# Performance work log

Measured on AMD Instinct MI355X. Metric: run time of the kernel, lower is better.

## Reference

```python
import jax, jax.numpy as jnp
import numpy as np

N, F, H, C, E = 100000, 512, 128, 8, 1600000
GAMMA = 1.0
EPS = 1e-8


def _xavier(key, shape):
    a = np.sqrt(6.0 / (shape[0] + shape[1])).astype(np.float32)
    return jax.random.uniform(key, shape, jnp.float32, -a, a)


def _agg(w, x, src, dst):
    # y[i] = sum_{e: dst[e]==i} w[e] * x[src[e]]  (sparse adj @ x)
    return jax.ops.segment_sum(w[:, None] * x[src], dst, num_segments=N)


def setup_inputs() -> dict:
    key = jax.random.key(0)
    ks = jax.random.split(key, 8)
    features = jax.random.normal(ks[0], (N, F), jnp.float32)
    edge_src = jax.random.randint(ks[1], (E,), 0, N)
    edge_dst = jax.random.randint(ks[2], (E,), 0, N)
    # degree-based normalized edge weights, mimicking D^p A D^p
    deg = jnp.zeros((N,), jnp.float32).at[edge_dst].add(1.0)
    deg = jnp.maximum(deg, 1.0)
    d_half = deg ** -0.5
    d_one = deg ** -1.0
    w1 = d_half[edge_dst] * d_half[edge_src]   # D^-1/2 A D^-1/2
    w2 = d_one[edge_dst] * d_one[edge_src]     # D^-1  A D^-1
    Wm1 = _xavier(ks[3], (F, H))
    Ws1 = _xavier(ks[4], (F, H))
    Wm2 = _xavier(ks[5], (H, C))
    Ws2 = _xavier(ks[6], (H, C))
    noise = jax.random.normal(ks[7], (N, C), jnp.float32)
    return {"features": features, "edge_src": edge_src, "edge_dst": edge_dst,
            "w1": w1, "w2": w2, "Wm1": Wm1, "Ws1": Ws1, "Wm2": Wm2,
            "Ws2": Ws2, "noise": noise}


def reference(features, edge_src, edge_dst, w1, w2, Wm1, Ws1, Wm2, Ws2, noise):
    # GGCL_F (eval mode: dropout is identity)
    miu1 = jax.nn.elu(features @ Wm1)
    sigma1 = jax.nn.relu(features @ Ws1)
    att1 = jnp.exp(-GAMMA * sigma1)
    miu_h = _agg(w1, miu1 * att1, edge_src, edge_dst)
    sigma_h = _agg(w2, sigma1 * att1 * att1, edge_src, edge_dst)
    # GGCL_D
    miu2 = jax.nn.elu(miu_h @ Wm2)
    sigma2 = jax.nn.relu(sigma_h @ Ws2)
    att2 = jnp.exp(-GAMMA * sigma2)
    mean_out = _agg(w1, miu2 * att2, edge_src, edge_dst)
    # GGCL_D returns (mean_out, sigma2); reparameterized sample
    return mean_out + noise * jnp.sqrt(sigma2 + EPS)
```

## Files before the change

### kernel.cpp

```cpp
#include <hip/hip_runtime.h>
#include <cstdint>

#define AS1 __attribute__((address_space(1)))
#define AS3 __attribute__((address_space(3)))

typedef __attribute__((ext_vector_type(8))) short short8;
typedef __attribute__((ext_vector_type(4))) float floatx4;
typedef unsigned short u16;

static constexpr int NN   = 100000;
static constexpr int FF   = 512;
static constexpr int HH   = 128;
static constexpr int EE   = 1600000;
static constexpr int PADM = 100096;
static constexpr int NPAD = 100352;
static constexpr int NB   = 98;

__device__ __forceinline__ u16 f2bf_rne(float v) {
    uint32_t u = __builtin_bit_cast(uint32_t, v);
    u += 0x7fffu + ((u >> 16) & 1u);
    return (u16)(u >> 16);
}
__device__ __forceinline__ float bf2f(u16 h) {
    uint32_t u = ((uint32_t)h) << 16;
    return __builtin_bit_cast(float, u);
}
__device__ __forceinline__ void async16(const void* g, void* l) {
    __builtin_amdgcn_global_load_lds((AS1 const void*)g, (AS3 void*)l, 16, 0, 0);
}

__global__ void k_split_w(const float* __restrict__ Wm1, const float* __restrict__ Ws1,
                          u16* __restrict__ whi, u16* __restrict__ wlo) {
    int t = blockIdx.x * 256 + threadIdx.x;
    int n = t >> 9, k = t & 511;
    float v = (n < HH) ? Wm1[k * HH + n] : Ws1[k * HH + (n - HH)];
    u16 h = f2bf_rne(v);
    whi[t] = h;
    wlo[t] = f2bf_rne(v - bf2f(h));
}

__global__ void k_prep_w2(const float* __restrict__ Wm2, const float* __restrict__ Ws2,
                          u16* __restrict__ W2B) {
    int t = blockIdx.x * 256 + threadIdx.x;
    int j = t & 7, l = (t >> 3) & 63, kc = (t >> 9) & 3, p = t >> 11;
    int n = l & 15, quad = l >> 4;
    int k = kc * 32 + quad * 8 + j;
    float v = 0.f;
    if (n < 8) {
        float wv = (p == 0) ? Wm2[k * 8 + n] : Ws2[k * 8 + n];
        v = (p == 2) ? (wv - bf2f(f2bf_rne(wv))) : wv;
    }
    W2B[t] = f2bf_rne(v);
}

__global__ void k_deg(const int* __restrict__ dst, int* __restrict__ deg) {
    int e = blockIdx.x * 256 + threadIdx.x;
    atomicAdd(&deg[dst[e]], 1);
}
__global__ void k_dh(const int* __restrict__ deg, float2* __restrict__ dd) {
    int t = blockIdx.x * 256 + threadIdx.x;
    int d = max(deg[t], 1);
    float df = (float)d;
    dd[t] = make_float2(1.f / sqrtf(df), 1.f / df);
}

__global__ __launch_bounds__(512, 4) void k_gemm(
        const float* __restrict__ A,
        const u16* __restrict__ BhiG, const u16* __restrict__ BloG,
        const u16* __restrict__ W2B, const float2* __restrict__ dd,
        float* __restrict__ Z) {
    __shared__ u16 sm[24576];
    const int tid = threadIdx.x;
    const int w = tid >> 6, lane = tid & 63;
    const int ml = lane & 15, quad = lane >> 4;
    const int wrow = w & 1, wcol = w >> 1;
    const int rowBase = blockIdx.x * 128;

    floatx4 am[4][2], as_[4][2];
#pragma unroll
    for (int i = 0; i < 4; i++)
#pragma unroll
        for (int j = 0; j < 2; j++) {
            am[i][j]  = (floatx4){0.f, 0.f, 0.f, 0.f};
            as_[i][j] = (floatx4){0.f, 0.f, 0.f, 0.f};
        }

    const int r0 = tid >> 2, ko = (tid & 3) * 8;
    const int arow = min(rowBase + r0, NN - 1);
    const float* gA = A + (size_t)arow * FF + ko;
    const u16* gBh = BhiG + (size_t)r0 * FF + ko;
    const u16* gBl = BloG + (size_t)(128 + r0) * FF + ko;

    const int aoff = (wrow * 64 + ml) * 32 + quad * 8;
    const int bmo  = 8192  + (32 * wcol + ml) * 32 + quad * 8;
    const int bso  = 12288 + (32 * wcol + ml) * 32 + quad * 8;
    const int blo_ = 16384 + (32 * wcol + ml) * 32 + quad * 8;

    for (int kt = 0; kt < FF; kt += 32) {
        __syncthreads();
        async16(gBh + kt,                      &sm[8192  + tid * 8]);
        async16(gBh + (size_t)128 * FF + kt,   &sm[12288 + tid * 8]);
        async16(gBl + kt,                      &sm[16384 + tid * 8]);
        {
            const float4* pA = (const float4*)(gA + kt);
            float4 x0 = pA[0], x1 = pA[1];
            float xv[8] = {x0.x, x0.y, x0.z, x0.w, x1.x, x1.y, x1.z, x1.w};
            short8 hv, lv;
#pragma unroll
            for (int q = 0; q < 8; q++) {
                u16 hh = f2bf_rne(xv[q]);
                hv[q] = (short)hh;
                lv[q] = (short)f2bf_rne(xv[q] - bf2f(hh));
            }
            *(short8*)&sm[tid * 8] = hv;
            *(short8*)&sm[4096 + tid * 8] = lv;
        }
        __syncthreads();

        short8 ah[4], al[4];
#pragma unroll
        for (int i = 0; i < 4; i++) ah[i] = *(const short8*)&sm[aoff + i * 512];
#pragma unroll
        for (int i = 0; i < 4; i++) al[i] = *(const short8*)&sm[4096 + aoff + i * 512];
#pragma unroll
        for (int jm = 0; jm < 2; jm++) {
            short8 b = *(const short8*)&sm[bmo + jm * 512];
#pragma unroll
            for (int i = 0; i < 4; i++)
                am[i][jm] = __builtin_amdgcn_mfma_f32_16x16x32_bf16(ah[i], b, am[i][jm], 0, 0, 0);
        }
#pragma unroll
        for (int js = 0; js < 2; js++) {
            short8 bh = *(const short8*)&sm[bso + js * 512];
            short8 bl = *(const short8*)&sm[blo_ + js * 512];
#pragma unroll
            for (int i = 0; i < 4; i++) {
                floatx4 c = as_[i][js];
                c = __builtin_amdgcn_mfma_f32_16x16x32_bf16(ah[i], bh, c, 0, 0, 0);
                c = __builtin_amdgcn_mfma_f32_16x16x32_bf16(ah[i], bl, c, 0, 0, 0);
                c = __builtin_amdgcn_mfma_f32_16x16x32_bf16(al[i], bh, c, 0, 0, 0);
                as_[i][js] = c;
            }
        }
    }

    short8 wm[4], wsh[4], wsl[4];
#pragma unroll
    for (int kc = 0; kc < 4; kc++) {
        wm[kc]  = *(const short8*)&W2B[(kc * 64 + lane) * 8];
        wsh[kc] = *(const short8*)&W2B[2048 + (kc * 64 + lane) * 8];
        wsl[kc] = *(const short8*)&W2B[4096 + (kc * 64 + lane) * 8];
    }
    const int rg = w & 1, pp = w >> 1;

#pragma unroll
    for (int h = 0; h < 4; h++) {
        __syncthreads();
        if (wrow == (h >> 1)) {
#pragma unroll
            for (int ii = 0; ii < 2; ii++) {
                int i = (h & 1) * 2 + ii;
#pragma unroll
                for (int jm = 0; jm < 2; jm++) {
                    int c = 32 * wcol + 16 * jm + ml;
#pragma unroll
                    for (int r = 0; r < 4; r++) {
                        int lr = ii * 16 + quad * 4 + r;
                        float2 d2 = dd[rowBase + h * 32 + lr];
                        float u = am[i][jm][r], v = as_[i][jm][r];
                        float m1 = u > 0.f ? u : __expf(u) - 1.f;
                        float s1 = v > 0.f ? v : 0.f;
                        float a1 = __expf(-s1);
                        float xmv = d2.x * m1 * a1;
                        float xsv = d2.y * s1 * a1 * a1;
                        u16 hh = f2bf_rne(xsv);
                        sm[lr * 136 + c]        = f2bf_rne(xmv);
                        sm[4352 + lr * 136 + c] = hh;
                        sm[8704 + lr * 136 + c] = f2bf_rne(xsv - bf2f(hh));
                    }
                }
            }
        }
        __syncthreads();
        if (w < 4) {
            floatx4 z = (floatx4){0.f, 0.f, 0.f, 0.f};
#pragma unroll
            for (int kc = 0; kc < 4; kc++) {
                if (pp == 0) {
                    short8 a = *(const short8*)&sm[(rg * 16 + ml) * 136 + kc * 32 + quad * 8];
                    z = __builtin_amdgcn_mfma_f32_16x16x32_bf16(a, wm[kc], z, 0, 0, 0);
                } else {
                    short8 a = *(const short8*)&sm[4352 + (rg * 16 + ml) * 136 + kc * 32 + quad * 8];
                    short8 b = *(const short8*)&sm[8704 + (rg * 16 + ml) * 136 + kc * 32 + quad * 8];
                    z = __builtin_amdgcn_mfma_f32_16x16x32_bf16(a, wsh[kc], z, 0, 0, 0);
                    z = __builtin_amdgcn_mfma_f32_16x16x32_bf16(a, wsl[kc], z, 0, 0, 0);
                    z = __builtin_amdgcn_mfma_f32_16x16x32_bf16(b, wsh[kc], z, 0, 0, 0);
                }
            }
            if (ml < 8) {
                int rowb = rowBase + h * 32 + rg * 16 + quad * 4;
#pragma unroll
                for (int r = 0; r < 4; r++)
                    if (rowb + r < NN) Z[(size_t)(rowb + r) * 16 + pp * 8 + ml] = z[r];
            }
        }
    }
}

__global__ void k_scan1(const int* __restrict__ deg, int* __restrict__ bsum) {
    int t = threadIdx.x;
    int4 v = ((const int4*)deg)[blockIdx.x * 256 + t];
    __shared__ int red[256];
    red[t] = v.x + v.y + v.z + v.w;
    __syncthreads();
    for (int o = 128; o > 0; o >>= 1) {
        if (t < o) red[t] += red[t + o];
        __syncthreads();
    }
    if (t == 0) bsum[blockIdx.x] = red[0];
}

__global__ void k_scan2(const int* __restrict__ bsum, int* __restrict__ boff) {
    int t = threadIdx.x;
    __shared__ int s[128];
    int own = (t < NB) ? bsum[t] : 0;
    s[t] = own;
    __syncthreads();
    for (int o = 1; o < 128; o <<= 1) {
        int v = (t >= o) ? s[t - o] : 0;
        __syncthreads();
        s[t] += v;
        __syncthreads();
    }
    if (t < NB) boff[t] = s[t] - own;
}

__global__ void k_scan3(const int* __restrict__ deg, const int* __restrict__ boff,
                        int* __restrict__ ptr, int* __restrict__ cursor) {
    int t = threadIdx.x;
    int gi = blockIdx.x * 256 + t;
    int4 v = ((const int4*)deg)[gi];
    int tsum = v.x + v.y + v.z + v.w;
    __shared__ int s[256];
    s[t] = tsum;
    __syncthreads();
    for (int o = 1; o < 256; o <<= 1) {
        int pv = (t >= o) ? s[t - o] : 0;
        __syncthreads();
        s[t] += pv;
        __syncthreads();
    }
    int base = boff[blockIdx.x] + (s[t] - tsum);
    int4 e;
    e.x = base;
    e.y = base + v.x;
    e.z = e.y + v.y;
    e.w = e.z + v.z;
    ((int4*)ptr)[gi] = e;
    ((int4*)cursor)[gi] = e;
}

__global__ void k_scatter(const int* __restrict__ src, const int* __restrict__ dst,
                          int* __restrict__ cursor, int* __restrict__ pay) {
    int e = blockIdx.x * 256 + threadIdx.x;
    int d = dst[e];
    int p = atomicAdd(&cursor[d], 1);
    int pr = pay[p];
    asm volatile("" :: "v"(pr) : "memory");
    pay[p] = src[e];
}

__global__ __launch_bounds__(256) void k_aggA(const int* __restrict__ ptr,
        const int* __restrict__ pay, const float* __restrict__ Z,
        const float2* __restrict__ dd, const float* __restrict__ noise,
        float* __restrict__ y, float* __restrict__ out) {
    int wave = threadIdx.x >> 6, lane = threadIdx.x & 63;
    int i = blockIdx.x * 4 + wave;
    if (i >= NN) return;
    int er = lane >> 3, c = lane & 7;
    int s0 = ptr[i], e0 = ptr[i + 1];
    float am = 0.f, as_ = 0.f;
    int j = s0 + er;
    int sidx = (j < e0) ? pay[j] : -1;
    while (sidx >= 0) {
        int jn = j + 8;
        int snext = (jn < e0) ? pay[jn] : -1;
        const float* zr = Z + (size_t)sidx * 16;
        am  += zr[c];
        as_ += zr[8 + c];
        j = jn;
        sidx = snext;
    }
    am  += __shfl_xor(am, 8, 64);
    am  += __shfl_xor(am, 16, 64);
    am  += __shfl_xor(am, 32, 64);
    as_ += __shfl_xor(as_, 8, 64);
    as_ += __shfl_xor(as_, 16, 64);
    as_ += __shfl_xor(as_, 32, 64);
    if (lane < 8) {
        float2 d2 = dd[i];
        float hm = d2.x * am, hs = d2.y * as_;
        float miu2 = hm > 0.f ? hm : __expf(hm) - 1.f;
        float s2 = hs > 0.f ? hs : 0.f;
        y[i * 8 + lane]   = d2.x * miu2 * __expf(-s2);
        out[i * 8 + lane] = noise[i * 8 + lane] * sqrtf(s2 + 1e-8f);
    }
}

__global__ __launch_bounds__(256) void k_aggB(const int* __restrict__ ptr,
        const int* __restrict__ pay, const float* __restrict__ y,
        const float2* __restrict__ dd, float* __restrict__ out) {
    int wave = threadIdx.x >> 6, lane = threadIdx.x & 63;
    int i = blockIdx.x * 4 + wave;
    if (i >= NN) return;
    int er = lane >> 3, c = lane & 7;
    int s0 = ptr[i], e0 = ptr[i + 1];
    float acc = 0.f;
    int j = s0 + er;
    int sidx = (j < e0) ? pay[j] : -1;
    while (sidx >= 0) {
        int jn = j + 8;
        int snext = (jn < e0) ? pay[jn] : -1;
        acc += y[(size_t)sidx * 8 + c];
        j = jn;
        sidx = snext;
    }
    acc += __shfl_xor(acc, 8, 64);
    acc += __shfl_xor(acc, 16, 64);
    acc += __shfl_xor(acc, 32, 64);
    if (lane < 8) out[i * 8 + lane] += dd[i].x * acc;
}

extern "C" void kernel_launch(void* const* d_in, const int* in_sizes, int n_in,
                              void* d_out, int out_size, void* d_ws, size_t ws_size,
                              hipStream_t stream) {
    (void)in_sizes; (void)n_in; (void)out_size; (void)ws_size;
    const float* feat  = (const float*)d_in[0];
    const int*   esrc  = (const int*)d_in[1];
    const int*   edst  = (const int*)d_in[2];
    const float* Wm1   = (const float*)d_in[5];
    const float* Ws1   = (const float*)d_in[6];
    const float* Wm2   = (const float*)d_in[7];
    const float* Ws2   = (const float*)d_in[8];
    const float* noise = (const float*)d_in[9];
    float* out = (float*)d_out;

    char* ws = (char*)d_ws;
    size_t off = 0;
    auto alloc = [&](size_t bytes) -> void* {
        void* p = ws + off;
        off += (bytes + 255) & ~(size_t)255;
        return p;
    };
    u16*    WhiT = (u16*)alloc((size_t)256 * 512 * 2);
    u16*    WloT = (u16*)alloc((size_t)256 * 512 * 2);
    u16*    W2B  = (u16*)alloc((size_t)6144 * 2);
    float*  Z    = (float*)alloc((size_t)NN * 16 * 4);
    float*  yb   = (float*)alloc((size_t)NN * 8 * 4);
    int*    deg  = (int*)alloc((size_t)NPAD * 4);
    float2* dd   = (float2*)alloc((size_t)NPAD * 8);
    int*    ptr  = (int*)alloc((size_t)(NPAD + 4) * 4);
    int*    cur  = (int*)alloc((size_t)NPAD * 4);
    int*    bsum = (int*)alloc(256 * 4);
    int*    boff = (int*)alloc(256 * 4);
    int*    pay  = (int*)alloc((size_t)EE * 4);

    hipMemsetAsync(deg, 0, (size_t)NPAD * 4, stream);

    k_deg    <<<EE / 256, 256, 0, stream>>>(edst, deg);
    k_dh     <<<NPAD / 256, 256, 0, stream>>>(deg, dd);
    k_scan1  <<<NB, 256, 0, stream>>>(deg, bsum);
    k_scan2  <<<1, 128, 0, stream>>>(bsum, boff);
    k_scan3  <<<NB, 256, 0, stream>>>(deg, boff, ptr, cur);
    k_scatter<<<EE / 256, 256, 0, stream>>>(esrc, edst, cur, pay);

    k_split_w<<<512, 256, 0, stream>>>(Wm1, Ws1, WhiT, WloT);
    k_prep_w2<<<24, 256, 0, stream>>>(Wm2, Ws2, W2B);
    k_gemm   <<<PADM / 128, 512, 0, stream>>>(feat, WhiT, WloT, W2B, dd, Z);

    k_aggA<<<(NN + 3) / 4, 256, 0, stream>>>(ptr, pay, Z, dd, noise, yb, out);
    k_aggB<<<(NN + 3) / 4, 256, 0, stream>>>(ptr, pay, yb, dd, out);
}
```

Before: 601.3 us.

## Double-buffer GEMM LDS tiles and XOR-swizzle layout to avoid bank conflicts

The first-layer GEMM main loop now double-buffers its LDS tiles. It prefetches the next K-slice of A into registers and issues async B loads into the alternate buffer while MFMAs run on the current buffer, then drops one barrier per iteration. It also XOR-swizzles the 8-element column chunks in LDS to reduce bank conflicts on the short8 reads. LDS use grows from 48KB to 80KB per block, which may reduce occupancy under the 512x4 launch bound.

Result: slower. 634.1 us (+5.5%).

```diff
diff --git a/kernel.cpp b/kernel.cpp
--- a/kernel.cpp
+++ b/kernel.cpp
@@ -27,6 +27,18 @@
 }
 __device__ __forceinline__ void async16(const void* g, void* l) {
     __builtin_amdgcn_global_load_lds((AS1 const void*)g, (AS3 void*)l, 16, 0, 0);
+}
+__device__ __forceinline__ void cvt_store(float4 x0, float4 x1, u16* dh, u16* dl) {
+    float xv[8] = {x0.x, x0.y, x0.z, x0.w, x1.x, x1.y, x1.z, x1.w};
+    short8 hv, lv;
+#pragma unroll
+    for (int q = 0; q < 8; q++) {
+        u16 hh = f2bf_rne(xv[q]);
+        hv[q] = (short)hh;
+        lv[q] = (short)f2bf_rne(xv[q] - bf2f(hh));
+    }
+    *(short8*)dh = hv;
+    *(short8*)dl = lv;
 }
 
 __global__ void k_split_w(const float* __restrict__ Wm1, const float* __restrict__ Ws1,
@@ -69,7 +81,7 @@
         const u16* __restrict__ BhiG, const u16* __restrict__ BloG,
         const u16* __restrict__ W2B, const float2* __restrict__ dd,
         float* __restrict__ Z) {
-    __shared__ u16 sm[24576];
+    __shared__ u16 sm[40960];
     const int tid = threadIdx.x;
     const int w = tid >> 6, lane = tid & 63;
     const int ml = lane & 15, quad = lane >> 4;
@@ -85,54 +97,63 @@
             as_[i][j] = (floatx4){0.f, 0.f, 0.f, 0.f};
         }
 
-    const int r0 = tid >> 2, ko = (tid & 3) * 8;
+    const int r0 = tid >> 2, q0 = tid & 3;
+    const int key0 = (r0 >> 1) & 3;
+    const int ko  = q0 * 8;
+    const int kob = (q0 ^ key0) * 8;
     const int arow = min(rowBase + r0, NN - 1);
     const float* gA = A + (size_t)arow * FF + ko;
-    const u16* gBh = BhiG + (size_t)r0 * FF + ko;
-    const u16* gBl = BloG + (size_t)(128 + r0) * FF + ko;
-
-    const int aoff = (wrow * 64 + ml) * 32 + quad * 8;
-    const int bmo  = 8192  + (32 * wcol + ml) * 32 + quad * 8;
-    const int bso  = 12288 + (32 * wcol + ml) * 32 + quad * 8;
-    const int blo_ = 16384 + (32 * wcol + ml) * 32 + quad * 8;
-
+    const u16* gBh = BhiG + (size_t)r0 * FF + kob;
+    const u16* gBl = BloG + (size_t)(128 + r0) * FF + kob;
+
+    const int awr = r0 * 32 + (q0 ^ key0) * 8;
+
+    const int xq = (ml >> 1) & 3;
+    const int aoff = (wrow * 64 + ml) * 32 + (quad ^ xq) * 8;
+    const int bmo  = 8192  + (32 * wcol + ml) * 32 + (quad ^ xq) * 8;
+    const int bso  = 12288 + (32 * wcol + ml) * 32 + (quad ^ xq) * 8;
+    const int blo_ = 16384 + (32 * wcol + ml) * 32 + (quad ^ xq) * 8;
+
+    float4 pf0, pf1;
+    {
+        const float4* pA = (const float4*)gA;
+        pf0 = pA[0]; pf1 = pA[1];
+        async16(gBh,                      &sm[8192  + tid * 8]);
+        async16(gBh + (size_t)128 * FF,   &sm[12288 + tid * 8]);
+        async16(gBl,                      &sm[16384 + tid * 8]);
+        cvt_store(pf0, pf1, &sm[awr], &sm[4096 + awr]);
+    }
+
+    int cur = 0;
     for (int kt = 0; kt < FF; kt += 32) {
         __syncthreads();
-        async16(gBh + kt,                      &sm[8192  + tid * 8]);
-        async16(gBh + (size_t)128 * FF + kt,   &sm[12288 + tid * 8]);
-        async16(gBl + kt,                      &sm[16384 + tid * 8]);
-        {
-            const float4* pA = (const float4*)(gA + kt);
-            float4 x0 = pA[0], x1 = pA[1];
-            float xv[8] = {x0.x, x0.y, x0.z, x0.w, x1.x, x1.y, x1.z, x1.w};
-            short8 hv, lv;
-#pragma unroll
-            for (int q = 0; q < 8; q++) {
-                u16 hh = f2bf_rne(xv[q]);
-                hv[q] = (short)hh;
-                lv[q] = (short)f2bf_rne(xv[q] - bf2f(hh));
-            }
-            *(short8*)&sm[tid * 8] = hv;
-            *(short8*)&sm[4096 + tid * 8] = lv;
-        }
-        __syncthreads();
+        const int cb = cur * 20480;
+        const int nb = (cur ^ 1) * 20480;
+        const bool more = (kt + 32 < FF);
+        if (more) {
+            const float4* pA = (const float4*)(gA + kt + 32);
+            pf0 = pA[0]; pf1 = pA[1];
+            async16(gBh + kt + 32,                      &sm[nb + 8192  + tid * 8]);
+            async16(gBh + (size_t)128 * FF + kt + 32,   &sm[nb + 12288 + tid * 8]);
+            async16(gBl + kt + 32,                      &sm[nb + 16384 + tid * 8]);
+        }
 
         short8 ah[4], al[4];
 #pragma unroll
-        for (int i = 0; i < 4; i++) ah[i] = *(const short8*)&sm[aoff + i * 512];
-#pragma unroll
-        for (int i = 0; i < 4; i++) al[i] = *(const short8*)&sm[4096 + aoff + i * 512];
+        for (int i = 0; i < 4; i++) ah[i] = *(const short8*)&sm[cb + aoff + i * 512];
+#pragma unroll
+        for (int i = 0; i < 4; i++) al[i] = *(const short8*)&sm[cb + 4096 + aoff + i * 512];
 #pragma unroll
         for (int jm = 0; jm < 2; jm++) {
-            short8 b = *(const short8*)&sm[bmo + jm * 512];
+            short8 b = *(const short8*)&sm[cb + bmo + jm * 512];
 #pragma unroll
             for (int i = 0; i < 4; i++)
                 am[i][jm] = __builtin_amdgcn_mfma_f32_16x16x32_bf16(ah[i], b, am[i][jm], 0, 0, 0);
         }
 #pragma unroll
         for (int js = 0; js < 2; js++) {
-            short8 bh = *(const short8*)&sm[bso + js * 512];
-            short8 bl = *(const short8*)&sm[blo_ + js * 512];
+            short8 bh = *(const short8*)&sm[cb + bso + js * 512];
+            short8 bl = *(const short8*)&sm[cb + blo_ + js * 512];
 #pragma unroll
             for (int i = 0; i < 4; i++) {
                 floatx4 c = as_[i][js];
@@ -142,6 +163,10 @@
                 as_[i][js] = c;
             }
         }
+
+        if (more)
+            cvt_store(pf0, pf1, &sm[nb + awr], &sm[nb + 4096 + awr]);
+        cur ^= 1;
     }
 
     short8 wm[4], wsh[4], wsl[4];
```

## Record atomic rank in degree pass, fuse dd into scan, vectorize aggregation gathers

Applied to the files above, without the earlier changes.

The degree-counting pass now stores each edge's atomic return value as its rank, so the CSR scatter computes positions as ptr[dst]+rank without a second atomic pass and without the cursor array. The degree-normalization kernel is folded into the third scan kernel. Both aggregation kernels switch to 16-byte vector gathers with more edges processed in parallel per wave, followed by wider shuffle reductions. The rank buffer aliases Z, which is safe only because Z is written later by the GEMM.

Result: faster. 568.7 us (-5.4%).

```diff
diff --git a/kernel.cpp b/kernel.cpp
--- a/kernel.cpp
+++ b/kernel.cpp
@@ -53,15 +53,10 @@
     W2B[t] = f2bf_rne(v);
 }
 
-__global__ void k_deg(const int* __restrict__ dst, int* __restrict__ deg) {
+__global__ void k_deg(const int* __restrict__ dst, int* __restrict__ deg,
+                      int* __restrict__ rank) {
     int e = blockIdx.x * 256 + threadIdx.x;
-    atomicAdd(&deg[dst[e]], 1);
-}
-__global__ void k_dh(const int* __restrict__ deg, float2* __restrict__ dd) {
-    int t = blockIdx.x * 256 + threadIdx.x;
-    int d = max(deg[t], 1);
-    float df = (float)d;
-    dd[t] = make_float2(1.f / sqrtf(df), 1.f / df);
+    rank[e] = atomicAdd(&deg[dst[e]], 1);
 }
 
 __global__ __launch_bounds__(512, 4) void k_gemm(
@@ -236,7 +231,7 @@
 }
 
 __global__ void k_scan3(const int* __restrict__ deg, const int* __restrict__ boff,
-                        int* __restrict__ ptr, int* __restrict__ cursor) {
+                        int* __restrict__ ptr, float2* __restrict__ dd) {
     int t = threadIdx.x;
     int gi = blockIdx.x * 256 + t;
     int4 v = ((const int4*)deg)[gi];
@@ -257,14 +252,20 @@
     e.z = e.y + v.y;
     e.w = e.z + v.z;
     ((int4*)ptr)[gi] = e;
-    ((int4*)cursor)[gi] = e;
+    float d0 = (float)max(v.x, 1), d1 = (float)max(v.y, 1);
+    float d2 = (float)max(v.z, 1), d3 = (float)max(v.w, 1);
+    float4 da = make_float4(1.f / sqrtf(d0), 1.f / d0, 1.f / sqrtf(d1), 1.f / d1);
+    float4 db = make_float4(1.f / sqrtf(d2), 1.f / d2, 1.f / sqrtf(d3), 1.f / d3);
+    ((float4*)dd)[gi * 2]     = da;
+    ((float4*)dd)[gi * 2 + 1] = db;
 }
 
 __global__ void k_scatter(const int* __restrict__ src, const int* __restrict__ dst,
-                          int* __restrict__ cursor, int* __restrict__ pay) {
+                          const int* __restrict__ rank, const int* __restrict__ ptr,
+                          int* __restrict__ pay) {
     int e = blockIdx.x * 256 + threadIdx.x;
     int d = dst[e];
-    int p = atomicAdd(&cursor[d], 1);
+    int p = ptr[d] + rank[e];
     int pr = pay[p];
     asm volatile("" :: "v"(pr) : "memory");
     pay[p] = src[e];
@@ -277,33 +278,42 @@
     int wave = threadIdx.x >> 6, lane = threadIdx.x & 63;
     int i = blockIdx.x * 4 + wave;
     if (i >= NN) return;
-    int er = lane >> 3, c = lane & 7;
+    int er = lane >> 2, q = lane & 3;
     int s0 = ptr[i], e0 = ptr[i + 1];
-    float am = 0.f, as_ = 0.f;
+    floatx4 acc = (floatx4){0.f, 0.f, 0.f, 0.f};
     int j = s0 + er;
     int sidx = (j < e0) ? pay[j] : -1;
     while (sidx >= 0) {
-        int jn = j + 8;
+        int jn = j + 16;
         int snext = (jn < e0) ? pay[jn] : -1;
-        const float* zr = Z + (size_t)sidx * 16;
-        am  += zr[c];
-        as_ += zr[8 + c];
+        floatx4 zv = *(const floatx4*)(Z + (size_t)sidx * 16 + q * 4);
+        acc += zv;
         j = jn;
         sidx = snext;
     }
-    am  += __shfl_xor(am, 8, 64);
-    am  += __shfl_xor(am, 16, 64);
-    am  += __shfl_xor(am, 32, 64);
-    as_ += __shfl_xor(as_, 8, 64);
-    as_ += __shfl_xor(as_, 16, 64);
-    as_ += __shfl_xor(as_, 32, 64);
-    if (lane < 8) {
+#pragma unroll
+    for (int m = 4; m <= 32; m <<= 1) {
+#pragma unroll
+        for (int k = 0; k < 4; k++) acc[k] += __shfl_xor(acc[k], m, 64);
+    }
+    floatx4 oth;
+#pragma unroll
+    for (int k = 0; k < 4; k++) oth[k] = __shfl_xor(acc[k], 2, 64);
+    if (lane < 2) {
         float2 d2 = dd[i];
-        float hm = d2.x * am, hs = d2.y * as_;
-        float miu2 = hm > 0.f ? hm : __expf(hm) - 1.f;
-        float s2 = hs > 0.f ? hs : 0.f;
-        y[i * 8 + lane]   = d2.x * miu2 * __expf(-s2);
-        out[i * 8 + lane] = noise[i * 8 + lane] * sqrtf(s2 + 1e-8f);
+        floatx4 nv = *(const floatx4*)(noise + (size_t)i * 8 + q * 4);
+        floatx4 yv, ov;
+#pragma unroll
+        for (int k = 0; k < 4; k++) {
+            float hm = d2.x * acc[k];
+            float hs = d2.y * oth[k];
+            float miu2 = hm > 0.f ? hm : __expf(hm) - 1.f;
+            float s2 = hs > 0.f ? hs : 0.f;
+            yv[k] = d2.x * miu2 * __expf(-s2);
+            ov[k] = nv[k] * sqrtf(s2 + 1e-8f);
+        }
+        *(floatx4*)(y + (size_t)i * 8 + q * 4)   = yv;
+        *(floatx4*)(out + (size_t)i * 8 + q * 4) = ov;
     }
 }
 
@@ -313,22 +323,32 @@
     int wave = threadIdx.x >> 6, lane = threadIdx.x & 63;
     int i = blockIdx.x * 4 + wave;
     if (i >= NN) return;
-    int er = lane >> 3, c = lane & 7;
+    int er = lane >> 1, q = lane & 1;
     int s0 = ptr[i], e0 = ptr[i + 1];
-    float acc = 0.f;
+    floatx4 acc = (floatx4){0.f, 0.f, 0.f, 0.f};
     int j = s0 + er;
     int sidx = (j < e0) ? pay[j] : -1;
     while (sidx >= 0) {
-        int jn = j + 8;
+        int jn = j + 32;
         int snext = (jn < e0) ? pay[jn] : -1;
-        acc += y[(size_t)sidx * 8 + c];
+        floatx4 yv = *(const floatx4*)(y + (size_t)sidx * 8 + q * 4);
+        acc += yv;
         j = jn;
         sidx = snext;
     }
-    acc += __shfl_xor(acc, 8, 64);
-    acc += __shfl_xor(acc, 16, 64);
-    acc += __shfl_xor(acc, 32, 64);
-    if (lane < 8) out[i * 8 + lane] += dd[i].x * acc;
+#pragma unroll
+    for (int m = 2; m <= 32; m <<= 1) {
+#pragma unroll
+        for (int k = 0; k < 4; k++) acc[k] += __shfl_xor(acc[k], m, 64);
+    }
+    if (lane < 2) {
+        float dh = dd[i].x;
+        float* po = out + (size_t)i * 8 + q * 4;
+        floatx4 o = *(floatx4*)po;
+#pragma unroll
+        for (int k = 0; k < 4; k++) o[k] += dh * acc[k];
+        *(floatx4*)po = o;
+    }
 }
 
 extern "C" void kernel_launch(void* const* d_in, const int* in_sizes, int n_in,
@@ -360,19 +380,18 @@
     int*    deg  = (int*)alloc((size_t)NPAD * 4);
     float2* dd   = (float2*)alloc((size_t)NPAD * 8);
     int*    ptr  = (int*)alloc((size_t)(NPAD + 4) * 4);
-    int*    cur  = (int*)alloc((size_t)NPAD * 4);
     int*    bsum = (int*)alloc(256 * 4);
     int*    boff = (int*)alloc(256 * 4);
     int*    pay  = (int*)alloc((size_t)EE * 4);
+    int*    rank = (int*)Z;
 
     hipMemsetAsync(deg, 0, (size_t)NPAD * 4, stream);
 
-    k_deg    <<<EE / 256, 256, 0, stream>>>(edst, deg);
-    k_dh     <<<NPAD / 256, 256, 0, stream>>>(deg, dd);
+    k_deg    <<<EE / 256, 256, 0, stream>>>(edst, deg, rank);
     k_scan1  <<<NB, 256, 0, stream>>>(deg, bsum);
     k_scan2  <<<1, 128, 0, stream>>>(bsum, boff);
-    k_scan3  <<<NB, 256, 0, stream>>>(deg, boff, ptr, cur);
-    k_scatter<<<EE / 256, 256, 0, stream>>>(esrc, edst, cur, pay);
+    k_scan3  <<<NB, 256, 0, stream>>>(deg, boff, ptr, dd);
+    k_scatter<<<EE / 256, 256, 0, stream>>>(esrc, edst, rank, ptr, pay);
 
     k_split_w<<<512, 256, 0, stream>>>(Wm1, Ws1, WhiT, WloT);
     k_prep_w2<<<24, 256, 0, stream>>>(Wm2, Ws2, W2B);
```
